# Performance work log

Hardware: AMD Instinct MI355X
Metric: run time of the kernel (lower is better)

Reference implementation:

```python
import jax, jax.numpy as jnp
import numpy as np

DIM = 192
QK_DIM = 192
WIN_S = 8
TOPK = 4


def setup_inputs() -> dict:
    key = jax.random.key(0)
    k1, k2, k3 = jax.random.split(key, 3)
    x = jax.random.normal(k1, (2, DIM, 256, 256), dtype=jnp.float32)
    # torch Linear default init ~ U(-1/sqrt(in), 1/sqrt(in)); scaled normal is fine as stand-in
    w_qkv = jax.random.normal(k2, (DIM, QK_DIM + QK_DIM + DIM), dtype=jnp.float32) * (DIM ** -0.5)
    b_qkv = jax.random.normal(k3, (QK_DIM + QK_DIM + DIM,), dtype=jnp.float32) * 0.01
    return {"x": x, "w_qkv": w_qkv, "b_qkv": b_qkv}


def reference(x, w_qkv, b_qkv):
    b, c, h, w = x.shape
    n_h, n_w = h // WIN_S, w // WIN_S
    hs, ws = h // n_h, w // n_w  # == WIN_S
    n_hw = n_h * n_w
    s_hw = hs * ws

    # b c h w -> b (n_h n_w) hs ws c
    xw = x.transpose(0, 2, 3, 1)                      # b h w c
    xw = xw.reshape(b, n_h, hs, n_w, ws, c)
    xw = xw.transpose(0, 1, 3, 2, 4, 5).reshape(b, n_hw, hs, ws, c)

    # QKVLinear: dim -> qk_dim + (qk_dim + dim)
    qkv = jnp.einsum('bnhwc,cd->bnhwd', xw, w_qkv) + b_qkv
    q = qkv[..., :QK_DIM]                             # (b, n_hw, hs, ws, qk_dim)
    kv = qkv[..., QK_DIM:]                            # (b, n_hw, hs, ws, qk_dim+dim)

    # WinProj 'mean'
    q_win = q.mean(axis=(2, 3))                       # (b, n_hw, qk_dim)
    k_win = kv[..., :QK_DIM].mean(axis=(2, 3))        # (b, n_hw, qk_dim)

    # TopkRouting (diff_routing=False -> detached; forward math identical)
    scale = QK_DIM ** -0.5
    logits = jnp.einsum('bnc,bmc->bnm', q_win * scale, k_win)  # (b, n_hw, n_hw)
    topk_logit, topk_idx = jax.lax.top_k(logits, TOPK)         # (b, n_hw, topk)
    r_weight = jax.nn.softmax(topk_logit, axis=-1)             # unused (mul_weight='none')

    # KVGather (mul_weight='none'): gather full kv pixel blocks of selected windows
    kv_pix = kv.reshape(b, n_hw, s_hw, QK_DIM + DIM)
    kv_pix_sel = jax.vmap(lambda kvb, idx: kvb[idx])(kv_pix, topk_idx)  # (b, n_hw, topk, s_hw, qk_dim+dim)

    v_pix_sel = kv_pix_sel[..., QK_DIM:]              # (b, n_hw, topk, s_hw, dim)
    return v_pix_sel
```

## Files before the change

### kernel.cpp

```cpp
#include <hip/hip_runtime.h>
#include <hip/hip_bf16.h>
#include <math.h>

#define NB   2
#define NC   192
#define HW   256
#define NWIN 1024
#define SHW  64
#define NDQ  192
#define WCOL 576

typedef short bf16x8 __attribute__((ext_vector_type(8)));
typedef float f32x4  __attribute__((ext_vector_type(4)));

__device__ inline unsigned int bf16pack(float a, float b) {
  unsigned int ua = __builtin_bit_cast(unsigned int, a);
  ua += 0x7fffu + ((ua >> 16) & 1u);
  unsigned int ub = __builtin_bit_cast(unsigned int, b);
  ub += 0x7fffu + ((ub >> 16) & 1u);
  return (ua >> 16) | (ub & 0xffff0000u);
}

__global__ __launch_bounds__(256) void k0_wvt(const float* __restrict__ w,
                                              unsigned short* __restrict__ wvt) {
  int id = blockIdx.x * 256 + threadIdx.x;
  int d = id / NC, c = id - d * NC;
  unsigned int u = __builtin_bit_cast(unsigned int, w[c * WCOL + 2 * NDQ + d]);
  u += 0x7fffu + ((u >> 16) & 1u);
  wvt[d * NC + c] = (unsigned short)(u >> 16);
}

__global__ __launch_bounds__(256) void k1_mean(const float* __restrict__ x,
                                               float* __restrict__ xmean) {
  int id = blockIdx.x * 256 + threadIdx.x;
  int n  = id & 1023;
  int c  = (id >> 10) % NC;
  int b  = id / (NC * NWIN);
  int wh = n >> 5, ww = n & 31;
  const float* p = x + (((size_t)(b * NC + c) * HW + wh * 8) * HW + ww * 8);
  double s = 0.0;
#pragma unroll
  for (int r = 0; r < 8; ++r) {
    float4 a = *(const float4*)(p + r * HW);
    float4 q = *(const float4*)(p + r * HW + 4);
    s += (double)a.x + a.y + a.z + a.w + q.x + q.y + q.z + q.w;
  }
  xmean[(size_t)(b * NWIN + n) * NC + c] = (float)(s * (1.0 / 64.0));
}

__global__ __launch_bounds__(192) void k2_qk(const float* __restrict__ xmean,
                                             const float* __restrict__ w,
                                             const float* __restrict__ bias,
                                             float* __restrict__ qw,
                                             float* __restrict__ kwT) {
  int b = blockIdx.y, n = blockIdx.x;
  int d = threadIdx.x;
  __shared__ float xs[NC];
  xs[d] = xmean[(size_t)(b * NWIN + n) * NC + d];
  __syncthreads();
  double aq = 0.0, ak = 0.0;
  for (int c = 0; c < NC; ++c) {
    double xc = (double)xs[c];
    aq += xc * (double)w[c * WCOL + d];
    ak += xc * (double)w[c * WCOL + NDQ + d];
  }
  const float scale = 0.0721687836487032f;
  float qv = (float)aq + bias[d];
  float kv = (float)ak + bias[NDQ + d];
  qw[(size_t)(b * NWIN + n) * NC + d] = qv * scale;
  kwT[(size_t)b * NC * NWIN + (size_t)d * NWIN + n] = kv;
}

__global__ __launch_bounds__(512) void k3_topk(const float* __restrict__ qw,
                                               const float* __restrict__ kwT,
                                               int* __restrict__ topk) {
  int b = blockIdx.y, n0 = blockIdx.x * 8;
  int t = threadIdx.x;
  __shared__ float qs[8][NC];
  __shared__ float lg[8][NWIN];
#pragma unroll
  for (int i = 0; i < 3; ++i) {
    int l = i * 512 + t;
    int r = l / NC, c = l - r * NC;
    qs[r][c] = qw[(size_t)(b * NWIN + n0 + r) * NC + c];
  }
  __syncthreads();

  double acc[8][2];
#pragma unroll
  for (int r = 0; r < 8; ++r) { acc[r][0] = 0.0; acc[r][1] = 0.0; }

  const float* kb = kwT + (size_t)b * NC * NWIN;
#pragma unroll 2
  for (int c = 0; c < NC; ++c) {
    float2 kv = *(const float2*)(kb + (size_t)c * NWIN + t * 2);
    double k0 = (double)kv.x, k1 = (double)kv.y;
#pragma unroll
    for (int r = 0; r < 8; ++r) {
      double q = (double)qs[r][c];
      acc[r][0] += q * k0;
      acc[r][1] += q * k1;
    }
  }
#pragma unroll
  for (int r = 0; r < 8; ++r) {
    lg[r][t * 2]     = (float)acc[r][0];
    lg[r][t * 2 + 1] = (float)acc[r][1];
  }
  __syncthreads();

  int wave = t >> 6, lane = t & 63;
  int r = wave;
  float v4[4];
  int   i4[4];
#pragma unroll
  for (int j = 0; j < 4; ++j) { v4[j] = -INFINITY; i4[j] = 0x7fffffff; }
  for (int i = 0; i < 16; ++i) {
    int idx = i * 64 + lane;
    float v = lg[r][idx];
    if (v > v4[3] || (v == v4[3] && idx < i4[3])) {
      v4[3] = v; i4[3] = idx;
#pragma unroll
      for (int j = 3; j > 0; --j) {
        if (v4[j] > v4[j-1] || (v4[j] == v4[j-1] && i4[j] < i4[j-1])) {
          float tv = v4[j]; v4[j] = v4[j-1]; v4[j-1] = tv;
          int ti = i4[j]; i4[j] = i4[j-1]; i4[j-1] = ti;
        }
      }
    }
  }
  for (int m = 1; m < 64; m <<= 1) {
    float ov[4]; int oi[4];
#pragma unroll
    for (int j = 0; j < 4; ++j) { ov[j] = __shfl_xor(v4[j], m); oi[j] = __shfl_xor(i4[j], m); }
    float nv[4]; int ni[4];
    int ia = 0, ib = 0;
#pragma unroll
    for (int j = 0; j < 4; ++j) {
      bool ta = (v4[ia] > ov[ib]) || (v4[ia] == ov[ib] && i4[ia] < oi[ib]);
      if (ta) { nv[j] = v4[ia]; ni[j] = i4[ia]; ++ia; }
      else    { nv[j] = ov[ib]; ni[j] = oi[ib]; ++ib; }
    }
#pragma unroll
    for (int j = 0; j < 4; ++j) { v4[j] = nv[j]; i4[j] = ni[j]; }
  }
  if (lane == 0) {
    int n = n0 + r;
#pragma unroll
    for (int k = 0; k < 4; ++k)
      topk[(size_t)(b * NWIN + n) * 4 + k] = i4[k];
  }
}

__global__ __launch_bounds__(1024) void kA_vgemm(const float* __restrict__ x,
                                                 const unsigned short* __restrict__ wvt,
                                                 const float* __restrict__ bias,
                                                 float* __restrict__ vtmp) {
  int b = blockIdx.y, g = blockIdx.x;
  int m0 = g * 4;
  int wh = m0 >> 5, ww0 = m0 & 31;
  int t = threadIdx.x;

  __shared__ unsigned short Xs[16384];

  int L = t & 63, wv = t >> 6;
  int win = wv >> 2, dq = wv & 3;
  int col = L & 15, kg = L >> 4;

  f32x4 acc[4][3];
#pragma unroll
  for (int dt = 0; dt < 3; ++dt) {
    float bv = bias[2 * NDQ + dq * 48 + dt * 16 + col];
    f32x4 bi = {bv, bv, bv, bv};
#pragma unroll
    for (int pt = 0; pt < 4; ++pt) acc[pt][dt] = bi;
  }

  int cp = t & 15, gi = t >> 4;
  int r = gi >> 3, w4 = gi & 7;
  int winS = w4 >> 1;
  int pS = r * 8 + (w4 & 1) * 4;
  const float* xb = x + (size_t)(b * NC) * (HW * HW) + (size_t)(wh * 8 + r) * HW + ww0 * 8 + w4 * 4;

  for (int cc = 0; cc < 6; ++cc) {
    const float* pl = xb + (size_t)(cc * 32 + cp * 2) * (HW * HW);
    float4 va = *(const float4*)pl;
    float4 vb = *(const float4*)(pl + HW * HW);
    float fa[4] = {va.x, va.y, va.z, va.w};
    float fb[4] = {vb.x, vb.y, vb.z, vb.w};
#pragma unroll
    for (int i = 0; i < 4; ++i) {
      int p = pS + i;
      unsigned int pk = bf16pack(fa[i], fb[i]);
      *(unsigned int*)((char*)Xs + (winS * 8192 + p * 128 + ((cp * 4) ^ ((p & 7) << 4)))) = pk;
    }
    __syncthreads();

    bf16x8 Bf[3];
#pragma unroll
    for (int dt = 0; dt < 3; ++dt)
      Bf[dt] = *(const bf16x8*)(wvt + (size_t)(dq * 48 + dt * 16 + col) * NC + cc * 32 + kg * 8);

#pragma unroll
    for (int pt = 0; pt < 4; ++pt) {
      int p = pt * 16 + col;
      bf16x8 Af = *(const bf16x8*)((const char*)Xs +
                    (win * 8192 + p * 128 + ((kg * 16) ^ ((p & 7) << 4))));
      acc[pt][0] = __builtin_amdgcn_mfma_f32_16x16x32_bf16(Af, Bf[0], acc[pt][0], 0, 0, 0);
      acc[pt][1] = __builtin_amdgcn_mfma_f32_16x16x32_bf16(Af, Bf[1], acc[pt][1], 0, 0, 0);
      acc[pt][2] = __builtin_amdgcn_mfma_f32_16x16x32_bf16(Af, Bf[2], acc[pt][2], 0, 0, 0);
    }
    __syncthreads();
  }

  float* dst = vtmp + (size_t)(b * NWIN + m0 + win) * (SHW * NC) + dq * 48 + col;
#pragma unroll
  for (int pt = 0; pt < 4; ++pt) {
#pragma unroll
    for (int rr = 0; rr < 4; ++rr) {
      float* dp = dst + (size_t)(pt * 16 + kg * 4 + rr) * NC;
      dp[0]  = acc[pt][0][rr];
      dp[16] = acc[pt][1][rr];
      dp[32] = acc[pt][2][rr];
    }
  }
}

__global__ __launch_bounds__(256) void kB_gather(const float* __restrict__ vtmp,
                                                 const int* __restrict__ topk,
                                                 float* __restrict__ out) {
  int id = blockIdx.x;
  int b = id >> 12;
  int m = topk[id];
  const float4* src = (const float4*)(vtmp + (size_t)(b * NWIN + m) * (SHW * NC));
  float4* dst = (float4*)(out + (size_t)id * (SHW * NC));
  int t = threadIdx.x;
#pragma unroll
  for (int i = 0; i < 12; ++i)
    dst[t + i * 256] = src[t + i * 256];
}

extern "C" void kernel_launch(void* const* d_in, const int* in_sizes, int n_in,
                              void* d_out, int out_size, void* d_ws, size_t ws_size,
                              hipStream_t stream) {
  const float* x    = (const float*)d_in[0];
  const float* w    = (const float*)d_in[1];
  const float* bias = (const float*)d_in[2];
  float* out = (float*)d_out;

  float* vtmp  = (float*)d_ws;
  float* xmean = vtmp + (size_t)100663296;
  float* qw    = xmean + 393216;
  float* kwT   = qw + 393216;
  int*   topk  = (int*)(kwT + 393216);
  unsigned short* wvt = (unsigned short*)(topk + 8192);

  k0_wvt<<<144, 256, 0, stream>>>(w, wvt);
  k1_mean<<<1536, 256, 0, stream>>>(x, xmean);
  k2_qk<<<dim3(1024, 2), 192, 0, stream>>>(xmean, w, bias, qw, kwT);
  k3_topk<<<dim3(128, 2), 512, 0, stream>>>(qw, kwT, topk);
  kA_vgemm<<<dim3(256, 2), 1024, 0, stream>>>(x, wvt, bias, vtmp);
  kB_gather<<<8192, 256, 0, stream>>>(vtmp, topk, out);
}
```

Measured before the change: 280.7 us.

## Fuse V projection GEMM into gather, recomputing per selected window slot

Replaces the separate V GEMM (writing a full fp32 vtmp buffer) and the gather copy kernel with one kernel per output slot. Each slot reads its top-k window's x block, projects it with MFMA and writes straight to the output. This removes the vtmp write and re-read, about 100 MB of traffic, at the cost of recomputing each window's projection about four times on average and re-reading x per slot.

```diff
diff --git a/kernel.cpp b/kernel.cpp
--- a/kernel.cpp
+++ b/kernel.cpp
@@ -152,50 +152,55 @@
   }
 }
 
-__global__ __launch_bounds__(1024) void kA_vgemm(const float* __restrict__ x,
-                                                 const unsigned short* __restrict__ wvt,
-                                                 const float* __restrict__ bias,
-                                                 float* __restrict__ vtmp) {
-  int b = blockIdx.y, g = blockIdx.x;
-  int m0 = g * 4;
-  int wh = m0 >> 5, ww0 = m0 & 31;
+__global__ __launch_bounds__(256) void kC_slot(const float* __restrict__ x,
+                                               const unsigned short* __restrict__ wvt,
+                                               const float* __restrict__ bias,
+                                               const int* __restrict__ topk,
+                                               float* __restrict__ out) {
+  int id = blockIdx.x;
+  int b = id >> 12;
+  int m = topk[id];
+  int wh = m >> 5, ww = m & 31;
   int t = threadIdx.x;
 
-  __shared__ unsigned short Xs[16384];
-
-  int L = t & 63, wv = t >> 6;
-  int win = wv >> 2, dq = wv & 3;
-  int col = L & 15, kg = L >> 4;
-
-  f32x4 acc[4][3];
-#pragma unroll
-  for (int dt = 0; dt < 3; ++dt) {
-    float bv = bias[2 * NDQ + dq * 48 + dt * 16 + col];
-    f32x4 bi = {bv, bv, bv, bv};
-#pragma unroll
-    for (int pt = 0; pt < 4; ++pt) acc[pt][dt] = bi;
-  }
-
-  int cp = t & 15, gi = t >> 4;
-  int r = gi >> 3, w4 = gi & 7;
-  int winS = w4 >> 1;
-  int pS = r * 8 + (w4 & 1) * 4;
-  const float* xb = x + (size_t)(b * NC) * (HW * HW) + (size_t)(wh * 8 + r) * HW + ww0 * 8 + w4 * 4;
-
-  for (int cc = 0; cc < 6; ++cc) {
-    const float* pl = xb + (size_t)(cc * 32 + cp * 2) * (HW * HW);
+  __shared__ unsigned short Xs[12288];
+
+  const float* xb = x + (size_t)(b * NC) * (HW * HW) + (size_t)(wh * 8) * HW + ww * 8;
+#pragma unroll
+  for (int i = 0; i < 6; ++i) {
+    int u = i * 256 + t;
+    int cp = u >> 4;
+    int q  = u & 15;
+    int rw = q >> 1, c4 = q & 1;
+    const float* pl = xb + (size_t)(2 * cp) * (HW * HW) + rw * HW + c4 * 4;
     float4 va = *(const float4*)pl;
     float4 vb = *(const float4*)(pl + HW * HW);
     float fa[4] = {va.x, va.y, va.z, va.w};
     float fb[4] = {vb.x, vb.y, vb.z, vb.w};
 #pragma unroll
-    for (int i = 0; i < 4; ++i) {
-      int p = pS + i;
-      unsigned int pk = bf16pack(fa[i], fb[i]);
-      *(unsigned int*)((char*)Xs + (winS * 8192 + p * 128 + ((cp * 4) ^ ((p & 7) << 4)))) = pk;
-    }
-    __syncthreads();
-
+    for (int k = 0; k < 4; ++k) {
+      int p = rw * 8 + c4 * 4 + k;
+      unsigned int pk = bf16pack(fa[k], fb[k]);
+      *(unsigned int*)((char*)Xs + (p * 384 + ((cp * 4) ^ ((p & 7) << 4)))) = pk;
+    }
+  }
+
+  int L = t & 63, dq = t >> 6;
+  int col = L & 15, kg = L >> 4;
+
+  f32x4 acc[4][3];
+#pragma unroll
+  for (int dt = 0; dt < 3; ++dt) {
+    float bv = bias[2 * NDQ + dq * 48 + dt * 16 + col];
+    f32x4 bi = {bv, bv, bv, bv};
+#pragma unroll
+    for (int pt = 0; pt < 4; ++pt) acc[pt][dt] = bi;
+  }
+
+  __syncthreads();
+
+#pragma unroll
+  for (int cc = 0; cc < 6; ++cc) {
     bf16x8 Bf[3];
 #pragma unroll
     for (int dt = 0; dt < 3; ++dt)
@@ -205,15 +210,14 @@
     for (int pt = 0; pt < 4; ++pt) {
       int p = pt * 16 + col;
       bf16x8 Af = *(const bf16x8*)((const char*)Xs +
-                    (win * 8192 + p * 128 + ((kg * 16) ^ ((p & 7) << 4))));
+                    (p * 384 + ((cc * 64 + kg * 16) ^ ((p & 7) << 4))));
       acc[pt][0] = __builtin_amdgcn_mfma_f32_16x16x32_bf16(Af, Bf[0], acc[pt][0], 0, 0, 0);
       acc[pt][1] = __builtin_amdgcn_mfma_f32_16x16x32_bf16(Af, Bf[1], acc[pt][1], 0, 0, 0);
       acc[pt][2] = __builtin_amdgcn_mfma_f32_16x16x32_bf16(Af, Bf[2], acc[pt][2], 0, 0, 0);
     }
-    __syncthreads();
-  }
-
-  float* dst = vtmp + (size_t)(b * NWIN + m0 + win) * (SHW * NC) + dq * 48 + col;
+  }
+
+  float* dst = out + (size_t)id * (SHW * NC) + dq * 48 + col;
 #pragma unroll
   for (int pt = 0; pt < 4; ++pt) {
 #pragma unroll
@@ -224,20 +228,6 @@
       dp[32] = acc[pt][2][rr];
     }
   }
-}
-
-__global__ __launch_bounds__(256) void kB_gather(const float* __restrict__ vtmp,
-                                                 const int* __restrict__ topk,
-                                                 float* __restrict__ out) {
-  int id = blockIdx.x;
-  int b = id >> 12;
-  int m = topk[id];
-  const float4* src = (const float4*)(vtmp + (size_t)(b * NWIN + m) * (SHW * NC));
-  float4* dst = (float4*)(out + (size_t)id * (SHW * NC));
-  int t = threadIdx.x;
-#pragma unroll
-  for (int i = 0; i < 12; ++i)
-    dst[t + i * 256] = src[t + i * 256];
 }
 
 extern "C" void kernel_launch(void* const* d_in, const int* in_sizes, int n_in,
@@ -248,8 +238,7 @@
   const float* bias = (const float*)d_in[2];
   float* out = (float*)d_out;
 
-  float* vtmp  = (float*)d_ws;
-  float* xmean = vtmp + (size_t)100663296;
+  float* xmean = (float*)d_ws;
   float* qw    = xmean + 393216;
   float* kwT   = qw + 393216;
   int*   topk  = (int*)(kwT + 393216);
@@ -259,6 +248,5 @@
   k1_mean<<<1536, 256, 0, stream>>>(x, xmean);
   k2_qk<<<dim3(1024, 2), 192, 0, stream>>>(xmean, w, bias, qw, kwT);
   k3_topk<<<dim3(128, 2), 512, 0, stream>>>(qw, kwT, topk);
-  kA_vgemm<<<dim3(256, 2), 1024, 0, stream>>>(x, wvt, bias, vtmp);
-  kB_gather<<<8192, 256, 0, stream>>>(vtmp, topk, out);
-}
+  kC_slot<<<8192, 256, 0, stream>>>(x, wvt, bias, topk, out);
+}
```

Result: slower. 357.3 us (+27.3%).
